# Performance work log

Hardware: AMD Instinct MI355X
Metric: run time of the kernel (lower is better)

## Reference

```python
import jax, jax.numpy as jnp
import numpy as np
import math

D_MODEL = 512
N_HEADS = 8
D_K = D_MODEL // N_HEADS
N_SAMPLES = 16
BETA = 1.0
SCALE = 1.0 / math.sqrt(D_K)
PROPOSAL_TEMP = 0.5


def setup_inputs() -> dict:
    key = jax.random.key(0)
    ks = jax.random.split(key, 9)
    B, S = 2, 512
    x = jax.random.normal(ks[0], (B, S, D_MODEL), dtype=jnp.float32)
    init = lambda k: jax.random.normal(k, (D_MODEL, D_MODEL), dtype=jnp.float32) * 0.02
    return {
        "x": x,
        "Wq": init(ks[1]), "bq": jnp.zeros((D_MODEL,), jnp.float32),
        "Wk": init(ks[2]), "bk": jnp.zeros((D_MODEL,), jnp.float32),
        "Wv": init(ks[3]), "bv": jnp.zeros((D_MODEL,), jnp.float32),
        "Wo": init(ks[4]), "bo": jnp.zeros((D_MODEL,), jnp.float32),
    }


def _importance_sampled_weights(scores):
    # scores: [B,H,S,S]. Replicates the per-row Python loop, fully vectorized.
    B, H, Sq, Sk = scores.shape
    target = jax.nn.softmax(scores * BETA, axis=-1)            # [B,H,Sq,Sk]
    # optimal proposal: 0.5*target + 0.5*uniform
    prop = PROPOSAL_TEMP * target + (1.0 - PROPOSAL_TEMP) / Sk
    R = B * H * Sq
    tf = target.reshape(R, Sk)
    pf = prop.reshape(R, Sk)
    # tsu_backend.sample_binary_layer(log(p/(1-p))) == Bernoulli(p) sampling
    s = jax.random.bernoulli(jax.random.key(42), pf[:, None, :], (R, N_SAMPLES, Sk))
    # importance weight = prod(target[sel]) / (prod(prop[sel]) * prod(1-prop[~sel]))
    pt = jnp.prod(jnp.where(s, tf[:, None, :], 1.0), axis=-1)                 # [R,N]
    pp = jnp.prod(jnp.where(s, pf[:, None, :], 1.0 - pf[:, None, :]), axis=-1)
    valid = (s.sum(-1) > 0) & (pp > 0)
    w = jnp.where(valid, pt / jnp.maximum(pp, 1e-38), 0.0)
    ws = w.sum(-1, keepdims=True)
    w = jnp.where(ws > 0, w / jnp.maximum(ws, 1e-38), 1.0 / N_SAMPLES)        # [R,N]
    wa = jnp.einsum('rn,rnk->rk', w, s.astype(jnp.float32))                   # [R,Sk]
    was = wa.sum(-1, keepdims=True)
    wa = jnp.where(was > 0, wa / jnp.maximum(was, 1e-38), 1.0 / Sk)
    return wa.reshape(B, H, Sq, Sk)


def reference(x, Wq, bq, Wk, bk, Wv, bv, Wo, bo):
    B, S, Dm = x.shape
    proj = lambda W, b: (x @ W + b).reshape(B, S, N_HEADS, D_K).transpose(0, 2, 1, 3)
    Q = proj(Wq, bq)  # [B,H,S,dk]
    K = proj(Wk, bk)
    V = proj(Wv, bv)
    scores = jnp.einsum('bhqd,bhkd->bhqk', Q, K) * SCALE
    # torch builds weights via torch.tensor(...) which detaches => constant w.r.t. params
    attn = jax.lax.stop_gradient(_importance_sampled_weights(scores))
    out = jnp.einsum('bhqk,bhkd->bhqd', attn, V)
    out = out.transpose(0, 2, 1, 3).reshape(B, S, Dm)
    return out @ Wo + bo
```

## Files before the change

### kernel.cpp

```cpp
#include <hip/hip_runtime.h>
#include <cstdint>
#include <cstddef>


#define ROTL(x, r) __builtin_rotateleft32((x), (r))

#define QR8(s)                                                                \
  x0[0]+=x1[0];x0[1]+=x1[1];x0[2]+=x1[2];x0[3]+=x1[3];                        \
  x0[4]+=x1[4];x0[5]+=x1[5];x0[6]+=x1[6];x0[7]+=x1[7];                        \
  x1[0]=ROTL(x1[0],s);x1[1]=ROTL(x1[1],s);x1[2]=ROTL(x1[2],s);                \
  x1[3]=ROTL(x1[3],s);x1[4]=ROTL(x1[4],s);x1[5]=ROTL(x1[5],s);                \
  x1[6]=ROTL(x1[6],s);x1[7]=ROTL(x1[7],s);                                    \
  x1[0]^=x0[0];x1[1]^=x0[1];x1[2]^=x0[2];x1[3]^=x0[3];                        \
  x1[4]^=x0[4];x1[5]^=x0[5];x1[6]^=x0[6];x1[7]^=x0[7];
#define INJ8(X, Y)                                                            \
  x0[0]+=(X);x0[1]+=(X);x0[2]+=(X);x0[3]+=(X);                                \
  x0[4]+=(X);x0[5]+=(X);x0[6]+=(X);x0[7]+=(X);                                \
  x1[0]+=(Y);x1[1]+=(Y);x1[2]+=(Y);x1[3]+=(Y);                                \
  x1[4]+=(Y);x1[5]+=(Y);x1[6]+=(Y);x1[7]+=(Y);
#define INJ8Y(Y)                                                              \
  x1[0]+=(Y);x1[1]+=(Y);x1[2]+=(Y);x1[3]+=(Y);                                \
  x1[4]+=(Y);x1[5]+=(Y);x1[6]+=(Y);x1[7]+=(Y);

__global__ __launch_bounds__(256)
void qkv_gemm(const float* __restrict__ x,
              const float* __restrict__ Wq, const float* __restrict__ bq,
              const float* __restrict__ Wk, const float* __restrict__ bk,
              const float* __restrict__ Wv, const float* __restrict__ bv,
              const float* __restrict__ bo, float* __restrict__ outp,
              float* __restrict__ Qw, float* __restrict__ KTw,
              float* __restrict__ Vw) {
  const int tid = threadIdx.x;
  if (blockIdx.z == 3) {
    const int blk = blockIdx.y * 16 + blockIdx.x;
    const size_t base4 = (size_t)blk * 1024 + tid;
    const float4* bo4 = (const float4*)bo;
    float4* out4 = (float4*)outp;
#pragma unroll
    for (int i = 0; i < 4; ++i) {
      const size_t idx4 = base4 + (size_t)i * 256;
      out4[idx4] = bo4[idx4 & 127];
    }
    return;
  }
  const float* W; const float* bias; float* out;
  if (blockIdx.z == 0)      { W = Wq; bias = bq; out = Qw; }
  else if (blockIdx.z == 1) { W = Wk; bias = bk; out = KTw; }
  else                      { W = Wv; bias = bv; out = Vw; }

  __shared__ float At[32][68];
  __shared__ float Bs[32][64];
  const int tx = tid & 15, ty = tid >> 4;
  const int row0 = blockIdx.x * 64, col0 = blockIdx.y * 64;
  float acc[4][4] = {};

  for (int kk = 0; kk < 512; kk += 32) {
    const int ar = tid >> 2;
#pragma unroll
    for (int i = 0; i < 2; ++i) {
      const int kc = ((tid & 3) << 3) + (i << 2);
      const float4 a4 =
          *(const float4*)&x[(size_t)(row0 + ar) * 512 + kk + kc];
      At[kc + 0][ar] = a4.x; At[kc + 1][ar] = a4.y;
      At[kc + 2][ar] = a4.z; At[kc + 3][ar] = a4.w;
    }
#pragma unroll
    for (int i = 0; i < 2; ++i) {
      const int idx = tid + (i << 8);
      const int br = idx >> 4, bc = (idx & 15) << 2;
      *(float4*)&Bs[br][bc] =
          *(const float4*)&W[(size_t)(kk + br) * 512 + col0 + bc];
    }
    __syncthreads();
#pragma unroll
    for (int p = 0; p < 32; ++p) {
      const float4 a4 = *(const float4*)&At[p][ty << 2];
      const float4 b4 = *(const float4*)&Bs[p][tx << 2];
      acc[0][0] = fmaf(a4.x, b4.x, acc[0][0]); acc[0][1] = fmaf(a4.x, b4.y, acc[0][1]);
      acc[0][2] = fmaf(a4.x, b4.z, acc[0][2]); acc[0][3] = fmaf(a4.x, b4.w, acc[0][3]);
      acc[1][0] = fmaf(a4.y, b4.x, acc[1][0]); acc[1][1] = fmaf(a4.y, b4.y, acc[1][1]);
      acc[1][2] = fmaf(a4.y, b4.z, acc[1][2]); acc[1][3] = fmaf(a4.y, b4.w, acc[1][3]);
      acc[2][0] = fmaf(a4.z, b4.x, acc[2][0]); acc[2][1] = fmaf(a4.z, b4.y, acc[2][1]);
      acc[2][2] = fmaf(a4.z, b4.z, acc[2][2]); acc[2][3] = fmaf(a4.z, b4.w, acc[2][3]);
      acc[3][0] = fmaf(a4.w, b4.x, acc[3][0]); acc[3][1] = fmaf(a4.w, b4.y, acc[3][1]);
      acc[3][2] = fmaf(a4.w, b4.z, acc[3][2]); acc[3][3] = fmaf(a4.w, b4.w, acc[3][3]);
    }
    __syncthreads();
  }
  const bool isK = (blockIdx.z == 1);
#pragma unroll
  for (int i = 0; i < 4; ++i) {
    const int row = row0 + (ty << 2) + i;
    const int b = row >> 9, s = row & 511;
#pragma unroll
    for (int j = 0; j < 4; ++j) {
      const int col = col0 + (tx << 2) + j;
      const int h = col >> 6, d = col & 63;
      const float v = acc[i][j] + bias[col];
      if (isK)
        out[(((size_t)(b * 8 + h) * 64 + d) * 512) + s] = v;
      else
        out[(((size_t)(b * 8 + h) * 512 + s) * 64) + d] = v;
    }
  }
}

__global__ __launch_bounds__(256)
void fused_sample(const float* __restrict__ Q, const float* __restrict__ KT,
                  const float* __restrict__ V, const float* __restrict__ Wo,
                  float* __restrict__ outp) {
  const int r = blockIdx.x;
  const int bh = r >> 9, q = r & 511;
  const int b = r >> 12, h = (r >> 9) & 7;
  const int tid = threadIdx.x;
  __shared__ __align__(16) float qs[64];
  __shared__ float red[8];
  __shared__ float tf[512];
  __shared__ __align__(16) uint32_t pscu2[512];
  __shared__ float wa[512];
  __shared__ float wr[16];
  __shared__ float redc[8];
  __shared__ float psum[4][64];
  __shared__ float o_s[64];
  __shared__ int   list[512];
  __shared__ int   cnt;

  if (tid == 0) cnt = 0;
  if (tid < 64) qs[tid] = Q[((size_t)bh * 512 + q) * 64 + tid];
  __syncthreads();

  float sc[2];
#pragma unroll
  for (int ii = 0; ii < 2; ++ii) {
    const int k = tid + (ii << 8);
    const float* Kp = KT + (size_t)bh * 64 * 512 + k;
    float s = 0.f;
#pragma unroll
    for (int d4 = 0; d4 < 16; ++d4) {
      const float4 qv = ((const float4*)qs)[d4];
      const float k0 = Kp[(size_t)(d4 * 4 + 0) * 512];
      const float k1 = Kp[(size_t)(d4 * 4 + 1) * 512];
      const float k2 = Kp[(size_t)(d4 * 4 + 2) * 512];
      const float k3 = Kp[(size_t)(d4 * 4 + 3) * 512];
      s = fmaf(qv.x, k0, s); s = fmaf(qv.y, k1, s);
      s = fmaf(qv.z, k2, s); s = fmaf(qv.w, k3, s);
    }
    sc[ii] = s * 0.125f;
  }
  float mx = fmaxf(sc[0], sc[1]);
  for (int m = 1; m < 64; m <<= 1) mx = fmaxf(mx, __shfl_xor(mx, m));
  if ((tid & 63) == 0) red[tid >> 6] = mx;
  __syncthreads();
  const float rowmax = fmaxf(fmaxf(red[0], red[1]), fmaxf(red[2], red[3]));
  const float e0 = expf(sc[0] - rowmax);
  const float e1 = expf(sc[1] - rowmax);
  float ssum = e0 + e1;
  for (int m = 1; m < 64; m <<= 1) ssum += __shfl_xor(ssum, m);
  if ((tid & 63) == 0) red[4 + (tid >> 6)] = ssum;
  __syncthreads();
  const float tot = red[4] + red[5] + red[6] + red[7];
  const float t0 = e0 / tot, t1 = e1 / tot;
  tf[tid] = t0; tf[tid + 256] = t1;
  wa[tid] = 0.f; wa[tid + 256] = 0.f;
  {
    const float p0 = fmaf(0.5f, t0, 0.0009765625f);
    const float p1 = fmaf(0.5f, t1, 0.0009765625f);
    {
      const int k = tid;
      pscu2[(((k & 31) >> 2) << 6) + ((k >> 5) << 2) + (k & 3)] =
          ((uint32_t)ceilf(p0 * 8388608.0f)) << 9;
    }
    {
      const int k = tid + 256;
      pscu2[(((k & 31) >> 2) << 6) + ((k >> 5) << 2) + (k & 3)] =
          ((uint32_t)ceilf(p1 * 8388608.0f)) << 9;
    }
    float ql = (1.f - p0) * (1.f - p1);
    for (int m = 1; m < 64; m <<= 1) ql *= __shfl_xor(ql, m);
    if ((tid & 63) == 0) redc[4 + (tid >> 6)] = ql;
  }
  __syncthreads();
  const float Qrow = redc[4] * redc[5] * redc[6] * redc[7];

  const int n = tid >> 4, t = tid & 15;
  const int k0i = t << 5;
  const uint32_t cbase =
      (uint32_t)r * 8192u + (uint32_t)n * 512u + (uint32_t)k0i + 42u;
  uint32_t bits = 0u;
#pragma unroll
  for (int jb = 0; jb < 32; jb += 8) {
    uint32_t x0[8], x1[8];
#pragma unroll
    for (int i = 0; i < 8; ++i) {
      const uint32_t c = cbase + (uint32_t)(jb + i);
      x0[i] = c;
      x1[i] = ROTL(c, 13) ^ c;
    }
    QR8(15) QR8(26) QR8(6)
    INJ8(42u, 0x1BD11BF1u)
    QR8(17) QR8(29) QR8(16) QR8(24)
    INJ8(0x1BD11BF0u, 2u)
    QR8(13) QR8(15) QR8(26) QR8(6)
    INJ8Y(45u)
    QR8(17) QR8(29) QR8(16) QR8(24)
    INJ8(42u, 0x1BD11BF4u)
    QR8(13) QR8(15) QR8(26) QR8(6)
    INJ8(0x1BD11BF0u, 5u)
    const uint4 pA = *(const uint4*)&pscu2[((jb >> 2) << 6) + (t << 2)];
    const uint4 pB = *(const uint4*)&pscu2[(((jb >> 2) + 1) << 6) + (t << 2)];
    bits |= (uint32_t)((x0[0] ^ x1[0]) < pA.x) << (jb + 0);
    bits |= (uint32_t)((x0[1] ^ x1[1]) < pA.y) << (jb + 1);
    bits |= (uint32_t)((x0[2] ^ x1[2]) < pA.z) << (jb + 2);
    bits |= (uint32_t)((x0[3] ^ x1[3]) < pA.w) << (jb + 3);
    bits |= (uint32_t)((x0[4] ^ x1[4]) < pB.x) << (jb + 4);
    bits |= (uint32_t)((x0[5] ^ x1[5]) < pB.y) << (jb + 5);
    bits |= (uint32_t)((x0[6] ^ x1[6]) < pB.z) << (jb + 6);
    bits |= (uint32_t)((x0[7] ^ x1[7]) < pB.w) << (jb + 7);
  }

  float ptl = 1.f, ratl = 1.f;
  int cl = __popc(bits);
  {
    uint32_t bb = bits;
    while (bb) {
      const int j = __builtin_ctz(bb);
      bb &= bb - 1u;
      const float tv = tf[k0i + j];
      const float p = fmaf(0.5f, tv, 0.0009765625f);
      ptl *= tv;
      ratl *= p / (1.f - p);
    }
  }
#pragma unroll
  for (int m = 1; m < 16; m <<= 1) {
    ptl *= __shfl_xor(ptl, m);
    ratl *= __shfl_xor(ratl, m);
    cl += __shfl_xor(cl, m);
  }
  if (t == 0) {
    const float pp = Qrow * ratl;
    wr[n] = (cl > 0 && pp > 0.f) ? (ptl / fmaxf(pp, 1e-38f)) : 0.f;
  }
  __syncthreads();
  float wsum = 0.f;
#pragma unroll
  for (int m2 = 0; m2 < 16; ++m2) wsum += wr[m2];
  const float wn = (wsum > 0.f) ? (wr[n] / fmaxf(wsum, 1e-38f)) : 0.0625f;
  {
    uint32_t bb = bits;
    while (bb) {
      const int j = __builtin_ctz(bb);
      bb &= bb - 1u;
      atomicAdd(&wa[k0i + j], wn);
    }
  }
  __syncthreads();

  float sp = wa[tid] + wa[tid + 256];
  for (int m = 1; m < 64; m <<= 1) sp += __shfl_xor(sp, m);
  if ((tid & 63) == 0) redc[tid >> 6] = sp;
  if (wa[tid] > 0.f)       { const int i = atomicAdd(&cnt, 1); list[i] = tid; }
  if (wa[tid + 256] > 0.f) { const int i = atomicAdd(&cnt, 1); list[i] = tid + 256; }
  __syncthreads();
  const float was = redc[0] + redc[1] + redc[2] + redc[3];
  const int nnz = cnt;

  const int g = tid >> 6, d = tid & 63;
  const float* Vb = V + ((size_t)(b * 8 + h) * 512) * 64;
  float acc = 0.f;
  if (was > 0.f) {
    const float inv = 1.f / fmaxf(was, 1e-38f);
    for (int i = g; i < nnz; i += 4) {
      const int k = list[i];
      acc = fmaf(wa[k] * inv, Vb[(size_t)k * 64 + d], acc);
    }
  } else {
    for (int k = g; k < 512; k += 4) acc += Vb[(size_t)k * 64 + d];
    acc *= 0.001953125f;
  }
  psum[g][d] = acc;
  __syncthreads();
  if (g == 0)
    o_s[d] = psum[0][d] + psum[1][d] + psum[2][d] + psum[3][d];
  __syncthreads();

  {
    const float* Wh = Wo + ((size_t)h * 64) * 512;
    float a0 = 0.f, a1 = 0.f;
#pragma unroll 8
    for (int dd = 0; dd < 64; ++dd) {
      const float ov = o_s[dd];
      a0 = fmaf(ov, Wh[(size_t)dd * 512 + tid], a0);
      a1 = fmaf(ov, Wh[(size_t)dd * 512 + tid + 256], a1);
    }
    float* orow = outp + ((size_t)(b * 512 + q)) * 512;
    atomicAdd(&orow[tid], a0);
    atomicAdd(&orow[tid + 256], a1);
  }
}

extern "C" void kernel_launch(void* const* d_in, const int* in_sizes, int n_in,
                              void* d_out, int out_size, void* d_ws,
                              size_t ws_size, hipStream_t stream) {
  const float* x  = (const float*)d_in[0];
  const float* Wq = (const float*)d_in[1];
  const float* bq = (const float*)d_in[2];
  const float* Wk = (const float*)d_in[3];
  const float* bk = (const float*)d_in[4];
  const float* Wv = (const float*)d_in[5];
  const float* bv = (const float*)d_in[6];
  const float* Wo = (const float*)d_in[7];
  const float* bo = (const float*)d_in[8];
  float* out = (float*)d_out;

  float* ws = (float*)d_ws;
  float* Qw = ws;
  float* KT = ws + 524288;
  float* Vw = ws + 1048576;

  dim3 gq(16, 8, 4);
  qkv_gemm<<<gq, 256, 0, stream>>>(x, Wq, bq, Wk, bk, Wv, bv, bo, out,
                                   Qw, KT, Vw);
  fused_sample<<<8192, 256, 0, stream>>>(Qw, KT, Vw, Wo, out);
}
```

Baseline: 254.3 us.

## Process four query rows per block to reuse K and Wo loads

Each block of fused_sample now handles four consecutive query rows of one head instead of one, so K columns and Wo rows loaded from global memory are reused across four rows in registers. The per-row softmax, sampling and weighted V accumulation run serially inside a loop, and the output projection accumulates four rows at once. This cuts global traffic for K and Wo and reduces block count, at the cost of less parallelism (2048 blocks) and longer serial per-block work, with more syncthreads per block.

```diff
diff --git a/kernel.cpp b/kernel.cpp
--- a/kernel.cpp
+++ b/kernel.cpp
@@ -109,11 +109,11 @@
 void fused_sample(const float* __restrict__ Q, const float* __restrict__ KT,
                   const float* __restrict__ V, const float* __restrict__ Wo,
                   float* __restrict__ outp) {
-  const int r = blockIdx.x;
-  const int bh = r >> 9, q = r & 511;
-  const int b = r >> 12, h = (r >> 9) & 7;
+  const int blk = blockIdx.x;
+  const int bh = blk >> 7, q0 = (blk & 127) << 2;
+  const int b = bh >> 3, h = bh & 7;
   const int tid = threadIdx.x;
-  __shared__ __align__(16) float qs[64];
+  __shared__ __align__(16) float qs[4][64];
   __shared__ float red[8];
   __shared__ float tf[512];
   __shared__ __align__(16) uint32_t pscu2[512];
@@ -121,181 +121,204 @@
   __shared__ float wr[16];
   __shared__ float redc[8];
   __shared__ float psum[4][64];
-  __shared__ float o_s[64];
+  __shared__ __align__(16) float o_t[64][4];
   __shared__ int   list[512];
   __shared__ int   cnt;
 
-  if (tid == 0) cnt = 0;
-  if (tid < 64) qs[tid] = Q[((size_t)bh * 512 + q) * 64 + tid];
+  qs[tid >> 6][tid & 63] =
+      Q[((size_t)bh * 512 + q0 + (tid >> 6)) * 64 + (tid & 63)];
   __syncthreads();
 
-  float sc[2];
+  float sc[4][2];
 #pragma unroll
   for (int ii = 0; ii < 2; ++ii) {
     const int k = tid + (ii << 8);
     const float* Kp = KT + (size_t)bh * 64 * 512 + k;
-    float s = 0.f;
+    float a0 = 0.f, a1 = 0.f, a2 = 0.f, a3 = 0.f;
 #pragma unroll
     for (int d4 = 0; d4 < 16; ++d4) {
-      const float4 qv = ((const float4*)qs)[d4];
+      const float4 v0 = ((const float4*)qs[0])[d4];
+      const float4 v1 = ((const float4*)qs[1])[d4];
+      const float4 v2 = ((const float4*)qs[2])[d4];
+      const float4 v3 = ((const float4*)qs[3])[d4];
       const float k0 = Kp[(size_t)(d4 * 4 + 0) * 512];
       const float k1 = Kp[(size_t)(d4 * 4 + 1) * 512];
       const float k2 = Kp[(size_t)(d4 * 4 + 2) * 512];
       const float k3 = Kp[(size_t)(d4 * 4 + 3) * 512];
-      s = fmaf(qv.x, k0, s); s = fmaf(qv.y, k1, s);
-      s = fmaf(qv.z, k2, s); s = fmaf(qv.w, k3, s);
-    }
-    sc[ii] = s * 0.125f;
-  }
-  float mx = fmaxf(sc[0], sc[1]);
-  for (int m = 1; m < 64; m <<= 1) mx = fmaxf(mx, __shfl_xor(mx, m));
-  if ((tid & 63) == 0) red[tid >> 6] = mx;
-  __syncthreads();
-  const float rowmax = fmaxf(fmaxf(red[0], red[1]), fmaxf(red[2], red[3]));
-  const float e0 = expf(sc[0] - rowmax);
-  const float e1 = expf(sc[1] - rowmax);
-  float ssum = e0 + e1;
-  for (int m = 1; m < 64; m <<= 1) ssum += __shfl_xor(ssum, m);
-  if ((tid & 63) == 0) red[4 + (tid >> 6)] = ssum;
-  __syncthreads();
-  const float tot = red[4] + red[5] + red[6] + red[7];
-  const float t0 = e0 / tot, t1 = e1 / tot;
-  tf[tid] = t0; tf[tid + 256] = t1;
-  wa[tid] = 0.f; wa[tid + 256] = 0.f;
-  {
-    const float p0 = fmaf(0.5f, t0, 0.0009765625f);
-    const float p1 = fmaf(0.5f, t1, 0.0009765625f);
-    {
-      const int k = tid;
-      pscu2[(((k & 31) >> 2) << 6) + ((k >> 5) << 2) + (k & 3)] =
-          ((uint32_t)ceilf(p0 * 8388608.0f)) << 9;
-    }
-    {
-      const int k = tid + 256;
-      pscu2[(((k & 31) >> 2) << 6) + ((k >> 5) << 2) + (k & 3)] =
-          ((uint32_t)ceilf(p1 * 8388608.0f)) << 9;
-    }
-    float ql = (1.f - p0) * (1.f - p1);
-    for (int m = 1; m < 64; m <<= 1) ql *= __shfl_xor(ql, m);
-    if ((tid & 63) == 0) redc[4 + (tid >> 6)] = ql;
-  }
-  __syncthreads();
-  const float Qrow = redc[4] * redc[5] * redc[6] * redc[7];
+      a0 = fmaf(v0.x, k0, a0); a0 = fmaf(v0.y, k1, a0);
+      a0 = fmaf(v0.z, k2, a0); a0 = fmaf(v0.w, k3, a0);
+      a1 = fmaf(v1.x, k0, a1); a1 = fmaf(v1.y, k1, a1);
+      a1 = fmaf(v1.z, k2, a1); a1 = fmaf(v1.w, k3, a1);
+      a2 = fmaf(v2.x, k0, a2); a2 = fmaf(v2.y, k1, a2);
+      a2 = fmaf(v2.z, k2, a2); a2 = fmaf(v2.w, k3, a2);
+      a3 = fmaf(v3.x, k0, a3); a3 = fmaf(v3.y, k1, a3);
+      a3 = fmaf(v3.z, k2, a3); a3 = fmaf(v3.w, k3, a3);
+    }
+    sc[0][ii] = a0 * 0.125f; sc[1][ii] = a1 * 0.125f;
+    sc[2][ii] = a2 * 0.125f; sc[3][ii] = a3 * 0.125f;
+  }
 
   const int n = tid >> 4, t = tid & 15;
   const int k0i = t << 5;
-  const uint32_t cbase =
-      (uint32_t)r * 8192u + (uint32_t)n * 512u + (uint32_t)k0i + 42u;
-  uint32_t bits = 0u;
-#pragma unroll
-  for (int jb = 0; jb < 32; jb += 8) {
-    uint32_t x0[8], x1[8];
-#pragma unroll
-    for (int i = 0; i < 8; ++i) {
-      const uint32_t c = cbase + (uint32_t)(jb + i);
-      x0[i] = c;
-      x1[i] = ROTL(c, 13) ^ c;
-    }
-    QR8(15) QR8(26) QR8(6)
-    INJ8(42u, 0x1BD11BF1u)
-    QR8(17) QR8(29) QR8(16) QR8(24)
-    INJ8(0x1BD11BF0u, 2u)
-    QR8(13) QR8(15) QR8(26) QR8(6)
-    INJ8Y(45u)
-    QR8(17) QR8(29) QR8(16) QR8(24)
-    INJ8(42u, 0x1BD11BF4u)
-    QR8(13) QR8(15) QR8(26) QR8(6)
-    INJ8(0x1BD11BF0u, 5u)
-    const uint4 pA = *(const uint4*)&pscu2[((jb >> 2) << 6) + (t << 2)];
-    const uint4 pB = *(const uint4*)&pscu2[(((jb >> 2) + 1) << 6) + (t << 2)];
-    bits |= (uint32_t)((x0[0] ^ x1[0]) < pA.x) << (jb + 0);
-    bits |= (uint32_t)((x0[1] ^ x1[1]) < pA.y) << (jb + 1);
-    bits |= (uint32_t)((x0[2] ^ x1[2]) < pA.z) << (jb + 2);
-    bits |= (uint32_t)((x0[3] ^ x1[3]) < pA.w) << (jb + 3);
-    bits |= (uint32_t)((x0[4] ^ x1[4]) < pB.x) << (jb + 4);
-    bits |= (uint32_t)((x0[5] ^ x1[5]) < pB.y) << (jb + 5);
-    bits |= (uint32_t)((x0[6] ^ x1[6]) < pB.z) << (jb + 6);
-    bits |= (uint32_t)((x0[7] ^ x1[7]) < pB.w) << (jb + 7);
-  }
-
-  float ptl = 1.f, ratl = 1.f;
-  int cl = __popc(bits);
-  {
-    uint32_t bb = bits;
-    while (bb) {
-      const int j = __builtin_ctz(bb);
-      bb &= bb - 1u;
-      const float tv = tf[k0i + j];
-      const float p = fmaf(0.5f, tv, 0.0009765625f);
-      ptl *= tv;
-      ratl *= p / (1.f - p);
-    }
-  }
-#pragma unroll
-  for (int m = 1; m < 16; m <<= 1) {
-    ptl *= __shfl_xor(ptl, m);
-    ratl *= __shfl_xor(ratl, m);
-    cl += __shfl_xor(cl, m);
-  }
-  if (t == 0) {
-    const float pp = Qrow * ratl;
-    wr[n] = (cl > 0 && pp > 0.f) ? (ptl / fmaxf(pp, 1e-38f)) : 0.f;
-  }
-  __syncthreads();
-  float wsum = 0.f;
-#pragma unroll
-  for (int m2 = 0; m2 < 16; ++m2) wsum += wr[m2];
-  const float wn = (wsum > 0.f) ? (wr[n] / fmaxf(wsum, 1e-38f)) : 0.0625f;
-  {
-    uint32_t bb = bits;
-    while (bb) {
-      const int j = __builtin_ctz(bb);
-      bb &= bb - 1u;
-      atomicAdd(&wa[k0i + j], wn);
-    }
-  }
-  __syncthreads();
-
-  float sp = wa[tid] + wa[tid + 256];
-  for (int m = 1; m < 64; m <<= 1) sp += __shfl_xor(sp, m);
-  if ((tid & 63) == 0) redc[tid >> 6] = sp;
-  if (wa[tid] > 0.f)       { const int i = atomicAdd(&cnt, 1); list[i] = tid; }
-  if (wa[tid + 256] > 0.f) { const int i = atomicAdd(&cnt, 1); list[i] = tid + 256; }
-  __syncthreads();
-  const float was = redc[0] + redc[1] + redc[2] + redc[3];
-  const int nnz = cnt;
-
   const int g = tid >> 6, d = tid & 63;
-  const float* Vb = V + ((size_t)(b * 8 + h) * 512) * 64;
-  float acc = 0.f;
-  if (was > 0.f) {
-    const float inv = 1.f / fmaxf(was, 1e-38f);
-    for (int i = g; i < nnz; i += 4) {
-      const int k = list[i];
-      acc = fmaf(wa[k] * inv, Vb[(size_t)k * 64 + d], acc);
-    }
-  } else {
-    for (int k = g; k < 512; k += 4) acc += Vb[(size_t)k * 64 + d];
-    acc *= 0.001953125f;
-  }
-  psum[g][d] = acc;
-  __syncthreads();
-  if (g == 0)
-    o_s[d] = psum[0][d] + psum[1][d] + psum[2][d] + psum[3][d];
+
+  for (int rr = 0; rr < 4; ++rr) {
+    const int r = bh * 512 + q0 + rr;
+    if (tid == 0) cnt = 0;
+    float mx = fmaxf(sc[rr][0], sc[rr][1]);
+    for (int m = 1; m < 64; m <<= 1) mx = fmaxf(mx, __shfl_xor(mx, m));
+    if ((tid & 63) == 0) red[tid >> 6] = mx;
+    __syncthreads();
+    const float rowmax = fmaxf(fmaxf(red[0], red[1]), fmaxf(red[2], red[3]));
+    const float e0 = expf(sc[rr][0] - rowmax);
+    const float e1 = expf(sc[rr][1] - rowmax);
+    float ssum = e0 + e1;
+    for (int m = 1; m < 64; m <<= 1) ssum += __shfl_xor(ssum, m);
+    if ((tid & 63) == 0) red[4 + (tid >> 6)] = ssum;
+    __syncthreads();
+    const float tot = red[4] + red[5] + red[6] + red[7];
+    const float t0 = e0 / tot, t1 = e1 / tot;
+    tf[tid] = t0; tf[tid + 256] = t1;
+    wa[tid] = 0.f; wa[tid + 256] = 0.f;
+    {
+      const float p0 = fmaf(0.5f, t0, 0.0009765625f);
+      const float p1 = fmaf(0.5f, t1, 0.0009765625f);
+      {
+        const int k = tid;
+        pscu2[(((k & 31) >> 2) << 6) + ((k >> 5) << 2) + (k & 3)] =
+            ((uint32_t)ceilf(p0 * 8388608.0f)) << 9;
+      }
+      {
+        const int k = tid + 256;
+        pscu2[(((k & 31) >> 2) << 6) + ((k >> 5) << 2) + (k & 3)] =
+            ((uint32_t)ceilf(p1 * 8388608.0f)) << 9;
+      }
+      float ql = (1.f - p0) * (1.f - p1);
+      for (int m = 1; m < 64; m <<= 1) ql *= __shfl_xor(ql, m);
+      if ((tid & 63) == 0) redc[4 + (tid >> 6)] = ql;
+    }
+    __syncthreads();
+    const float Qrow = redc[4] * redc[5] * redc[6] * redc[7];
+
+    const uint32_t cbase =
+        (uint32_t)r * 8192u + (uint32_t)n * 512u + (uint32_t)k0i + 42u;
+    uint32_t bits = 0u;
+#pragma unroll
+    for (int jb = 0; jb < 32; jb += 8) {
+      uint32_t x0[8], x1[8];
+#pragma unroll
+      for (int i = 0; i < 8; ++i) {
+        const uint32_t c = cbase + (uint32_t)(jb + i);
+        x0[i] = c;
+        x1[i] = ROTL(c, 13) ^ c;
+      }
+      QR8(15) QR8(26) QR8(6)
+      INJ8(42u, 0x1BD11BF1u)
+      QR8(17) QR8(29) QR8(16) QR8(24)
+      INJ8(0x1BD11BF0u, 2u)
+      QR8(13) QR8(15) QR8(26) QR8(6)
+      INJ8Y(45u)
+      QR8(17) QR8(29) QR8(16) QR8(24)
+      INJ8(42u, 0x1BD11BF4u)
+      QR8(13) QR8(15) QR8(26) QR8(6)
+      INJ8(0x1BD11BF0u, 5u)
+      const uint4 pA = *(const uint4*)&pscu2[((jb >> 2) << 6) + (t << 2)];
+      const uint4 pB = *(const uint4*)&pscu2[(((jb >> 2) + 1) << 6) + (t << 2)];
+      bits |= (uint32_t)((x0[0] ^ x1[0]) < pA.x) << (jb + 0);
+      bits |= (uint32_t)((x0[1] ^ x1[1]) < pA.y) << (jb + 1);
+      bits |= (uint32_t)((x0[2] ^ x1[2]) < pA.z) << (jb + 2);
+      bits |= (uint32_t)((x0[3] ^ x1[3]) < pA.w) << (jb + 3);
+      bits |= (uint32_t)((x0[4] ^ x1[4]) < pB.x) << (jb + 4);
+      bits |= (uint32_t)((x0[5] ^ x1[5]) < pB.y) << (jb + 5);
+      bits |= (uint32_t)((x0[6] ^ x1[6]) < pB.z) << (jb + 6);
+      bits |= (uint32_t)((x0[7] ^ x1[7]) < pB.w) << (jb + 7);
+    }
+
+    float ptl = 1.f, ratl = 1.f;
+    int cl = __popc(bits);
+    {
+      uint32_t bb = bits;
+      while (bb) {
+        const int j = __builtin_ctz(bb);
+        bb &= bb - 1u;
+        const float tv = tf[k0i + j];
+        const float p = fmaf(0.5f, tv, 0.0009765625f);
+        ptl *= tv;
+        ratl *= p / (1.f - p);
+      }
+    }
+#pragma unroll
+    for (int m = 1; m < 16; m <<= 1) {
+      ptl *= __shfl_xor(ptl, m);
+      ratl *= __shfl_xor(ratl, m);
+      cl += __shfl_xor(cl, m);
+    }
+    if (t == 0) {
+      const float pp = Qrow * ratl;
+      wr[n] = (cl > 0 && pp > 0.f) ? (ptl / fmaxf(pp, 1e-38f)) : 0.f;
+    }
+    __syncthreads();
+    float wsum = 0.f;
+#pragma unroll
+    for (int m2 = 0; m2 < 16; ++m2) wsum += wr[m2];
+    const float wn = (wsum > 0.f) ? (wr[n] / fmaxf(wsum, 1e-38f)) : 0.0625f;
+    {
+      uint32_t bb = bits;
+      while (bb) {
+        const int j = __builtin_ctz(bb);
+        bb &= bb - 1u;
+        atomicAdd(&wa[k0i + j], wn);
+      }
+    }
+    __syncthreads();
+
+    float sp = wa[tid] + wa[tid + 256];
+    for (int m = 1; m < 64; m <<= 1) sp += __shfl_xor(sp, m);
+    if ((tid & 63) == 0) redc[tid >> 6] = sp;
+    if (wa[tid] > 0.f)       { const int i = atomicAdd(&cnt, 1); list[i] = tid; }
+    if (wa[tid + 256] > 0.f) { const int i = atomicAdd(&cnt, 1); list[i] = tid + 256; }
+    __syncthreads();
+    const float was = redc[0] + redc[1] + redc[2] + redc[3];
+    const int nnz = cnt;
+
+    const float* Vb = V + ((size_t)(b * 8 + h) * 512) * 64;
+    float acc = 0.f;
+    if (was > 0.f) {
+      const float inv = 1.f / fmaxf(was, 1e-38f);
+      for (int i = g; i < nnz; i += 4) {
+        const int k = list[i];
+        acc = fmaf(wa[k] * inv, Vb[(size_t)k * 64 + d], acc);
+      }
+    } else {
+      for (int k = g; k < 512; k += 4) acc += Vb[(size_t)k * 64 + d];
+      acc *= 0.001953125f;
+    }
+    psum[g][d] = acc;
+    __syncthreads();
+    if (g == 0)
+      o_t[d][rr] = psum[0][d] + psum[1][d] + psum[2][d] + psum[3][d];
+  }
   __syncthreads();
 
   {
     const float* Wh = Wo + ((size_t)h * 64) * 512;
-    float a0 = 0.f, a1 = 0.f;
+    float a0[4] = {}, a1[4] = {};
 #pragma unroll 8
     for (int dd = 0; dd < 64; ++dd) {
-      const float ov = o_s[dd];
-      a0 = fmaf(ov, Wh[(size_t)dd * 512 + tid], a0);
-      a1 = fmaf(ov, Wh[(size_t)dd * 512 + tid + 256], a1);
-    }
-    float* orow = outp + ((size_t)(b * 512 + q)) * 512;
-    atomicAdd(&orow[tid], a0);
-    atomicAdd(&orow[tid + 256], a1);
+      const float4 ov = *(const float4*)&o_t[dd][0];
+      const float w0 = Wh[(size_t)dd * 512 + tid];
+      const float w1 = Wh[(size_t)dd * 512 + tid + 256];
+      a0[0] = fmaf(ov.x, w0, a0[0]); a1[0] = fmaf(ov.x, w1, a1[0]);
+      a0[1] = fmaf(ov.y, w0, a0[1]); a1[1] = fmaf(ov.y, w1, a1[1]);
+      a0[2] = fmaf(ov.z, w0, a0[2]); a1[2] = fmaf(ov.z, w1, a1[2]);
+      a0[3] = fmaf(ov.w, w0, a0[3]); a1[3] = fmaf(ov.w, w1, a1[3]);
+    }
+#pragma unroll
+    for (int rr = 0; rr < 4; ++rr) {
+      float* orow = outp + ((size_t)(b * 512 + q0 + rr)) * 512;
+      atomicAdd(&orow[tid], a0[rr]);
+      atomicAdd(&orow[tid + 256], a1[rr]);
+    }
   }
 }
 
@@ -321,5 +344,5 @@
   dim3 gq(16, 8, 4);
   qkv_gemm<<<gq, 256, 0, stream>>>(x, Wq, bq, Wk, bk, Wv, bv, bo, out,
                                    Qw, KT, Vw);
-  fused_sample<<<8192, 256, 0, stream>>>(Qw, KT, Vw, Wo, out);
+  fused_sample<<<2048, 256, 0, stream>>>(Qw, KT, Vw, Wo, out);
 }
```

After: 269.7 us. 1.06x slower.

## Precompute per-head V·Wo product so sampling kernel skips output projection

Applied to the files above, without the earlier changes.

The V-projection blocks now multiply their V tile by the head's slice of Wo and store a per-head [S,512] VW matrix. The sampling kernel then combines the sparse weights directly against VW rows, dropping the 64-wide intermediate, its shared-memory reduction and the per-row 64x512 Wo GEMV. This trades a large per-row output-projection cost for a bigger workspace (16x512x512 floats) and wider gathered rows per nonzero key, plus extra GEMM work in the first kernel.

```diff
diff --git a/kernel.cpp b/kernel.cpp
--- a/kernel.cpp
+++ b/kernel.cpp
@@ -27,9 +27,9 @@
               const float* __restrict__ Wq, const float* __restrict__ bq,
               const float* __restrict__ Wk, const float* __restrict__ bk,
               const float* __restrict__ Wv, const float* __restrict__ bv,
-              const float* __restrict__ bo, float* __restrict__ outp,
-              float* __restrict__ Qw, float* __restrict__ KTw,
-              float* __restrict__ Vw) {
+              const float* __restrict__ Wo, const float* __restrict__ bo,
+              float* __restrict__ outp, float* __restrict__ Qw,
+              float* __restrict__ KTw, float* __restrict__ VW) {
   const int tid = threadIdx.x;
   if (blockIdx.z == 3) {
     const int blk = blockIdx.y * 16 + blockIdx.x;
@@ -43,13 +43,15 @@
     }
     return;
   }
-  const float* W; const float* bias; float* out;
-  if (blockIdx.z == 0)      { W = Wq; bias = bq; out = Qw; }
-  else if (blockIdx.z == 1) { W = Wk; bias = bk; out = KTw; }
-  else                      { W = Wv; bias = bv; out = Vw; }
+  const float* W; const float* bias;
+  if (blockIdx.z == 0)      { W = Wq; bias = bq; }
+  else if (blockIdx.z == 1) { W = Wk; bias = bk; }
+  else                      { W = Wv; bias = bv; }
 
   __shared__ float At[32][68];
   __shared__ float Bs[32][64];
+  __shared__ __align__(16) float Vt[64][68];
+  __shared__ __align__(16) float Ws[64][33];
   const int tx = tid & 15, ty = tid >> 4;
   const int row0 = blockIdx.x * 64, col0 = blockIdx.y * 64;
   float acc[4][4] = {};
@@ -87,31 +89,83 @@
     }
     __syncthreads();
   }
-  const bool isK = (blockIdx.z == 1);
-#pragma unroll
-  for (int i = 0; i < 4; ++i) {
-    const int row = row0 + (ty << 2) + i;
-    const int b = row >> 9, s = row & 511;
-#pragma unroll
-    for (int j = 0; j < 4; ++j) {
-      const int col = col0 + (tx << 2) + j;
-      const int h = col >> 6, d = col & 63;
-      const float v = acc[i][j] + bias[col];
-      if (isK)
-        out[(((size_t)(b * 8 + h) * 64 + d) * 512) + s] = v;
-      else
-        out[(((size_t)(b * 8 + h) * 512 + s) * 64) + d] = v;
+
+  if (blockIdx.z == 0) {
+#pragma unroll
+    for (int i = 0; i < 4; ++i) {
+      const int row = row0 + (ty << 2) + i;
+      const int b = row >> 9, s = row & 511;
+#pragma unroll
+      for (int j = 0; j < 4; ++j) {
+        const int col = col0 + (tx << 2) + j;
+        const int h = col >> 6, d = col & 63;
+        Qw[(((size_t)(b * 8 + h) * 512 + s) * 64) + d] =
+            acc[i][j] + bias[col];
+      }
+    }
+  } else if (blockIdx.z == 1) {
+#pragma unroll
+    for (int i = 0; i < 4; ++i) {
+      const int row = row0 + (ty << 2) + i;
+      const int b = row >> 9, s = row & 511;
+#pragma unroll
+      for (int j = 0; j < 4; ++j) {
+        const int col = col0 + (tx << 2) + j;
+        const int h = col >> 6, d = col & 63;
+        KTw[(((size_t)(b * 8 + h) * 64 + d) * 512) + s] = acc[i][j] + bias[col];
+      }
+    }
+  } else {
+    const int h = blockIdx.y;
+    const int b = row0 >> 9, s0 = row0 & 511;
+    const int bh = b * 8 + h;
+#pragma unroll
+    for (int i = 0; i < 4; ++i) {
+#pragma unroll
+      for (int j = 0; j < 4; ++j) {
+        Vt[(ty << 2) + i][(tx << 2) + j] =
+            acc[i][j] + bias[col0 + (tx << 2) + j];
+      }
+    }
+    const int tx2 = tid & 7, ty2 = tid >> 3;
+    for (int cc = 0; cc < 512; cc += 32) {
+#pragma unroll
+      for (int i = 0; i < 2; ++i) {
+        const int slot = tid + (i << 8);
+        const int dr = slot >> 3, c4 = (slot & 7) << 2;
+        *(float4*)&Ws[dr][c4] =
+            *(const float4*)&Wo[(size_t)(h * 64 + dr) * 512 + cc + c4];
+      }
+      __syncthreads();
+      float a2[2][4] = {};
+#pragma unroll
+      for (int p = 0; p < 64; ++p) {
+        const float v0 = Vt[(ty2 << 1) + 0][p];
+        const float v1 = Vt[(ty2 << 1) + 1][p];
+        const float4 w4 = *(const float4*)&Ws[p][tx2 << 2];
+        a2[0][0] = fmaf(v0, w4.x, a2[0][0]); a2[0][1] = fmaf(v0, w4.y, a2[0][1]);
+        a2[0][2] = fmaf(v0, w4.z, a2[0][2]); a2[0][3] = fmaf(v0, w4.w, a2[0][3]);
+        a2[1][0] = fmaf(v1, w4.x, a2[1][0]); a2[1][1] = fmaf(v1, w4.y, a2[1][1]);
+        a2[1][2] = fmaf(v1, w4.z, a2[1][2]); a2[1][3] = fmaf(v1, w4.w, a2[1][3]);
+      }
+#pragma unroll
+      for (int i = 0; i < 2; ++i) {
+        float4 st; st.x = a2[i][0]; st.y = a2[i][1];
+        st.z = a2[i][2]; st.w = a2[i][3];
+        *(float4*)&VW[((size_t)(bh * 512 + s0 + (ty2 << 1) + i)) * 512 + cc +
+                      (tx2 << 2)] = st;
+      }
+      __syncthreads();
     }
   }
 }
 
 __global__ __launch_bounds__(256)
 void fused_sample(const float* __restrict__ Q, const float* __restrict__ KT,
-                  const float* __restrict__ V, const float* __restrict__ Wo,
-                  float* __restrict__ outp) {
+                  const float* __restrict__ VW, float* __restrict__ outp) {
   const int r = blockIdx.x;
   const int bh = r >> 9, q = r & 511;
-  const int b = r >> 12, h = (r >> 9) & 7;
+  const int b = r >> 12;
   const int tid = threadIdx.x;
   __shared__ __align__(16) float qs[64];
   __shared__ float red[8];
@@ -120,8 +174,6 @@
   __shared__ float wa[512];
   __shared__ float wr[16];
   __shared__ float redc[8];
-  __shared__ float psum[4][64];
-  __shared__ float o_s[64];
   __shared__ int   list[512];
   __shared__ int   cnt;
 
@@ -265,38 +317,26 @@
   const float was = redc[0] + redc[1] + redc[2] + redc[3];
   const int nnz = cnt;
 
-  const int g = tid >> 6, d = tid & 63;
-  const float* Vb = V + ((size_t)(b * 8 + h) * 512) * 64;
-  float acc = 0.f;
+  const float* VWb = VW + ((size_t)bh * 512) * 512;
+  float a0 = 0.f, a1 = 0.f;
   if (was > 0.f) {
     const float inv = 1.f / fmaxf(was, 1e-38f);
-    for (int i = g; i < nnz; i += 4) {
+    for (int i = 0; i < nnz; ++i) {
       const int k = list[i];
-      acc = fmaf(wa[k] * inv, Vb[(size_t)k * 64 + d], acc);
+      const float w = wa[k] * inv;
+      a0 = fmaf(w, VWb[(size_t)k * 512 + tid], a0);
+      a1 = fmaf(w, VWb[(size_t)k * 512 + tid + 256], a1);
     }
   } else {
-    for (int k = g; k < 512; k += 4) acc += Vb[(size_t)k * 64 + d];
-    acc *= 0.001953125f;
-  }
-  psum[g][d] = acc;
-  __syncthreads();
-  if (g == 0)
-    o_s[d] = psum[0][d] + psum[1][d] + psum[2][d] + psum[3][d];
-  __syncthreads();
-
-  {
-    const float* Wh = Wo + ((size_t)h * 64) * 512;
-    float a0 = 0.f, a1 = 0.f;
-#pragma unroll 8
-    for (int dd = 0; dd < 64; ++dd) {
-      const float ov = o_s[dd];
-      a0 = fmaf(ov, Wh[(size_t)dd * 512 + tid], a0);
-      a1 = fmaf(ov, Wh[(size_t)dd * 512 + tid + 256], a1);
-    }
-    float* orow = outp + ((size_t)(b * 512 + q)) * 512;
-    atomicAdd(&orow[tid], a0);
-    atomicAdd(&orow[tid + 256], a1);
-  }
+    for (int k = 0; k < 512; ++k) {
+      a0 += VWb[(size_t)k * 512 + tid];
+      a1 += VWb[(size_t)k * 512 + tid + 256];
+    }
+    a0 *= 0.001953125f; a1 *= 0.001953125f;
+  }
+  float* orow = outp + ((size_t)(b * 512 + q)) * 512;
+  atomicAdd(&orow[tid], a0);
+  atomicAdd(&orow[tid + 256], a1);
 }
 
 extern "C" void kernel_launch(void* const* d_in, const int* in_sizes, int n_in,
@@ -316,10 +356,10 @@
   float* ws = (float*)d_ws;
   float* Qw = ws;
   float* KT = ws + 524288;
-  float* Vw = ws + 1048576;
+  float* VW = ws + 1048576;
 
   dim3 gq(16, 8, 4);
-  qkv_gemm<<<gq, 256, 0, stream>>>(x, Wq, bq, Wk, bk, Wv, bv, bo, out,
-                                   Qw, KT, Vw);
-  fused_sample<<<8192, 256, 0, stream>>>(Qw, KT, Vw, Wo, out);
+  qkv_gemm<<<gq, 256, 0, stream>>>(x, Wq, bq, Wk, bk, Wv, bv, Wo, bo, out,
+                                   Qw, KT, VW);
+  fused_sample<<<8192, 256, 0, stream>>>(Qw, KT, VW, out);
 }
```

Measured after the change: 276.6 us. +8.8%, slower.
